# Kernel tuning notes

Measured on AMD Instinct MI355X. Metric: run time of the kernel, lower is better.

Reference implementation:

```python
import jax, jax.numpy as jnp
import numpy as np

INPUT_DIM = 768
HIDDEN_DIM = 256
ASPECT_NUM = 20
BATCH = 1024


def setup_inputs() -> dict:
    key = jax.random.key(0)
    k_x, k_w1, k_b1, k_w2, k_b2, k_id = jax.random.split(key, 6)
    X = jax.random.normal(k_x, (BATCH, INPUT_DIM), dtype=jnp.float32)
    aspect_ids = jax.random.randint(k_id, (BATCH,), 0, ASPECT_NUM, dtype=jnp.int64)
    # embedding tables (learned params), init like nn.Embedding (N(0,1))
    W1_embs = jax.random.normal(k_w1, (ASPECT_NUM, INPUT_DIM * HIDDEN_DIM), dtype=jnp.float32)
    b1_embs = jax.random.normal(k_b1, (ASPECT_NUM, HIDDEN_DIM), dtype=jnp.float32)
    W2_embs = jax.random.normal(k_w2, (ASPECT_NUM, HIDDEN_DIM * 2), dtype=jnp.float32)
    b2_embs = jax.random.normal(k_b2, (ASPECT_NUM, 2), dtype=jnp.float32)
    return {"X": X, "aspect_ids": aspect_ids, "W1_embs": W1_embs,
            "b1_embs": b1_embs, "W2_embs": W2_embs, "b2_embs": b2_embs}


def reference(X, aspect_ids, W1_embs, b1_embs, W2_embs, b2_embs):
    B = X.shape[0]
    # per-sample parameter gather (embedding lookup)
    W1 = W1_embs[aspect_ids].reshape(B, INPUT_DIM, HIDDEN_DIM)  # (B, D, H)
    b1 = b1_embs[aspect_ids]                                     # (B, H)
    W2 = W2_embs[aspect_ids].reshape(B, HIDDEN_DIM, 2)           # (B, H, 2)
    b2 = b2_embs[aspect_ids]                                     # (B, 2)
    # batched tiny 2-layer MLP
    out1 = jax.nn.relu(jnp.einsum('bd,bdh->bh', X, W1) + b1)     # (B, H)
    logits = jnp.einsum('bh,bht->bt', out1, W2) + b2             # (B, 2)
    return logits
```

## Files before the change

kernel.cpp:

```cpp
#include <hip/hip_runtime.h>


constexpr int D  = 768;
constexpr int H  = 256;
constexpr int NA = 20;
constexpr int NB = 1024;
constexpr int S  = 64;
constexpr int DKN = 8;
constexpr int KS  = D / DKN;
constexpr int HSN = 4;
constexpr int RW  = KS + 8;

constexpr size_t WS_NEEDED = (size_t)NB * DKN * H * 2;

typedef __attribute__((ext_vector_type(8))) short short8v;
typedef __attribute__((ext_vector_type(4))) float f32x4;

__device__ __forceinline__ unsigned f2bf(float x) {
    const unsigned u = __float_as_uint(x);
    return (u + 0x7FFFu + ((u >> 16) & 1u)) >> 16;
}
__device__ __forceinline__ float bflo(unsigned u) { return __uint_as_float(u << 16); }
__device__ __forceinline__ float bfhi(unsigned u) { return __uint_as_float(u & 0xFFFF0000u); }

__global__ __launch_bounds__(256, 4) void gemm1_kernel(
    const float* __restrict__ X,
    const int*   __restrict__ aids,
    const float* __restrict__ W1,
    const float* __restrict__ b1,
    unsigned short* __restrict__ part)
{
    __shared__ __align__(16) short w1t[64 * RW];
    __shared__ __align__(16) short xl[S * RW];
    __shared__ int sidx[NB + S];
    __shared__ int n_sh;

    const int t = threadIdx.x;
    const int w = t >> 6, l = t & 63;
    const int bid = blockIdx.x;
    const int hs  = bid / 160;
    const int p   = bid - hs * 160;
    const int aid = p % NA;
    const int dk  = p / NA;

    if (w == 0) {
        int run = 0;
        #pragma unroll
        for (int base = 0; base < NB; base += 256) {
            const int4 v = *reinterpret_cast<const int4*>(&aids[base + l * 4]);
            #pragma unroll
            for (int j = 0; j < 4; ++j) {
                const int id = (j == 0) ? v.x : (j == 1) ? v.y : (j == 2) ? v.z : v.w;
                const unsigned long long m = __ballot(id == aid);
                const int pre = run + __popcll(m & ((1ull << l) - 1));
                if (id == aid) sidx[pre] = base + l * 4 + j;
                run += __popcll(m);
            }
        }
        if (run > 0) {
            const int last = sidx[run - 1];
            const int npad = ((run + S - 1) / S) * S;
            if (run + l < npad) sidx[run + l] = last;
        }
        if (l == 0) n_sh = run;
    } else {
        const float* W1s = W1 + (size_t)aid * D * H + (size_t)dk * KS * H + hs * 64;
        unsigned* w1u = reinterpret_cast<unsigned*>(w1t);
        for (int i = t - 64; i < (KS / 2) * 16; i += 192) {
            const int kq = i >> 4, cq = i & 15;
            const int k0 = kq * 2;
            const float4 a = *reinterpret_cast<const float4*>(&W1s[(size_t)k0 * H + cq * 4]);
            const float4 b = *reinterpret_cast<const float4*>(&W1s[(size_t)(k0 + 1) * H + cq * 4]);
            w1u[(cq * 4 + 0) * (RW / 2) + kq] = f2bf(a.x) | (f2bf(b.x) << 16);
            w1u[(cq * 4 + 1) * (RW / 2) + kq] = f2bf(a.y) | (f2bf(b.y) << 16);
            w1u[(cq * 4 + 2) * (RW / 2) + kq] = f2bf(a.z) | (f2bf(b.z) << 16);
            w1u[(cq * 4 + 3) * (RW / 2) + kq] = f2bf(a.w) | (f2bf(b.w) << 16);
        }
    }
    __syncthreads();
    const int n = n_sh;
    if (n == 0) return;

    const int cg = l & 15, gq = l >> 4;
    const short* wa = &w1t[(w * 16 + cg) * RW + 8 * gq];
    const int gcol = hs * 64 + w * 16 + cg;
    const float b1v = (dk == 0) ? b1[(size_t)aid * H + gcol] : 0.f;

    for (int ch = 0; ch * S < n; ++ch) {
        for (int i = t; i < S * (KS / 4); i += 256) {
            const int r = i / (KS / 4), q = i - r * (KS / 4);
            const float4 v = *reinterpret_cast<const float4*>(
                &X[(size_t)sidx[ch * S + r] * D + dk * KS + q * 4]);
            uint2 o;
            o.x = f2bf(v.x) | (f2bf(v.y) << 16);
            o.y = f2bf(v.z) | (f2bf(v.w) << 16);
            *reinterpret_cast<uint2*>(&xl[r * RW + q * 4]) = o;
        }
        __syncthreads();

        f32x4 acc0 = {0,0,0,0}, acc1 = {0,0,0,0}, acc2 = {0,0,0,0}, acc3 = {0,0,0,0};
        #pragma unroll
        for (int ks = 0; ks < 3; ++ks) {
            const short8v bv = *reinterpret_cast<const short8v*>(wa + ks * 32);
            const int kof = ks * 32 + 8 * gq;
            acc0 = __builtin_amdgcn_mfma_f32_16x16x32_bf16(
                *reinterpret_cast<const short8v*>(&xl[(cg)      * RW + kof]), bv, acc0, 0, 0, 0);
            acc1 = __builtin_amdgcn_mfma_f32_16x16x32_bf16(
                *reinterpret_cast<const short8v*>(&xl[(16 + cg) * RW + kof]), bv, acc1, 0, 0, 0);
            acc2 = __builtin_amdgcn_mfma_f32_16x16x32_bf16(
                *reinterpret_cast<const short8v*>(&xl[(32 + cg) * RW + kof]), bv, acc2, 0, 0, 0);
            acc3 = __builtin_amdgcn_mfma_f32_16x16x32_bf16(
                *reinterpret_cast<const short8v*>(&xl[(48 + cg) * RW + kof]), bv, acc3, 0, 0, 0);
        }

        const int cv = min(S, n - ch * S);
        #pragma unroll
        for (int r = 0; r < 4; ++r) {
            const int s0 = gq * 4 + r;
            if (s0 < cv)
                part[((size_t)sidx[ch * S + s0] * DKN + dk) * H + gcol] =
                    (unsigned short)f2bf(acc0[r] + b1v);
            const int s1 = 16 + gq * 4 + r;
            if (s1 < cv)
                part[((size_t)sidx[ch * S + s1] * DKN + dk) * H + gcol] =
                    (unsigned short)f2bf(acc1[r] + b1v);
            const int s2 = 32 + gq * 4 + r;
            if (s2 < cv)
                part[((size_t)sidx[ch * S + s2] * DKN + dk) * H + gcol] =
                    (unsigned short)f2bf(acc2[r] + b1v);
            const int s3 = 48 + gq * 4 + r;
            if (s3 < cv)
                part[((size_t)sidx[ch * S + s3] * DKN + dk) * H + gcol] =
                    (unsigned short)f2bf(acc3[r] + b1v);
        }
        if ((ch + 1) * S < n) __syncthreads();
    }
}

__global__ __launch_bounds__(256) void finish_kernel(
    const int*            __restrict__ aids,
    const unsigned short* __restrict__ part,
    const float*          __restrict__ W2,
    const float*          __restrict__ b2,
    float*                __restrict__ out)
{
    const int w = threadIdx.x >> 6, l = threadIdx.x & 63;
    const int half = l >> 5;
    const int m = l & 31;
    const int s = blockIdx.x * 8 + w * 2 + half;
    const int aid = aids[s];

    const unsigned short* ps = part + (size_t)s * DKN * H + m * 8;
    float v[8] = {0, 0, 0, 0, 0, 0, 0, 0};
    #pragma unroll
    for (int dk = 0; dk < DKN; ++dk) {
        const uint4 r = *reinterpret_cast<const uint4*>(ps + dk * H);
        v[0] += bflo(r.x); v[1] += bfhi(r.x);
        v[2] += bflo(r.y); v[3] += bfhi(r.y);
        v[4] += bflo(r.z); v[5] += bfhi(r.z);
        v[6] += bflo(r.w); v[7] += bfhi(r.w);
    }

    const float4* W2v = reinterpret_cast<const float4*>(&W2[((size_t)aid * H + m * 8) * 2]);
    float p0 = 0.f, p1 = 0.f;
    #pragma unroll
    for (int c4 = 0; c4 < 4; ++c4) {
        const float4 wv = W2v[c4];
        const float o0 = fmaxf(v[c4 * 2 + 0], 0.f);
        const float o1 = fmaxf(v[c4 * 2 + 1], 0.f);
        p0 += o0 * wv.x + o1 * wv.z;
        p1 += o0 * wv.y + o1 * wv.w;
    }

    #pragma unroll
    for (int msk = 1; msk < 32; msk <<= 1) {
        p0 += __shfl_xor(p0, msk, 64);
        p1 += __shfl_xor(p1, msk, 64);
    }
    if (m == 0) {
        const float2 b2v = reinterpret_cast<const float2*>(b2)[aid];
        reinterpret_cast<float2*>(out)[s] = make_float2(p0 + b2v.x, p1 + b2v.y);
    }
}

__global__ __launch_bounds__(256, 4) void aspect_mlp_fallback(
    const float* __restrict__ X, const int* __restrict__ aspect_ids,
    const float* __restrict__ W1_embs, const float* __restrict__ b1_embs,
    const float* __restrict__ W2_embs, const float* __restrict__ b2_embs,
    float* __restrict__ out)
{
    __shared__ float xs[D];
    __shared__ float pl[4][H];
    __shared__ float red[4][2];
    const int b = blockIdx.x, t = threadIdx.x, w = t >> 6, l = t & 63;
    const int aid = aspect_ids[b];
    const float4* Xr = reinterpret_cast<const float4*>(X + (size_t)b * D);
    if (t < D / 4) reinterpret_cast<float4*>(xs)[t] = Xr[t];
    __syncthreads();
    const float4* W1v = reinterpret_cast<const float4*>(W1_embs + (size_t)aid * (D * H));
    float4 acc = make_float4(0.f, 0.f, 0.f, 0.f);
    const int d0 = w * (D / 4);
    for (int d = d0; d < d0 + D / 4; ++d) {
        const float xv = xs[d];
        const float4 wv = W1v[d * (H / 4) + l];
        acc.x = fmaf(xv, wv.x, acc.x); acc.y = fmaf(xv, wv.y, acc.y);
        acc.z = fmaf(xv, wv.z, acc.z); acc.w = fmaf(xv, wv.w, acc.w);
    }
    reinterpret_cast<float4*>(pl[w])[l] = acc;
    __syncthreads();
    const float o = fmaxf(pl[0][t] + pl[1][t] + pl[2][t] + pl[3][t] + b1_embs[aid * H + t], 0.f);
    const float2 w2 = reinterpret_cast<const float2*>(W2_embs)[aid * H + t];
    float p0 = o * w2.x, p1 = o * w2.y;
    for (int s = 32; s; s >>= 1) { p0 += __shfl_xor(p0, s, 64); p1 += __shfl_xor(p1, s, 64); }
    if (l == 0) { red[w][0] = p0; red[w][1] = p1; }
    __syncthreads();
    if (t == 0) {
        const float2 bias2 = reinterpret_cast<const float2*>(b2_embs)[aid];
        out[b * 2 + 0] = red[0][0] + red[1][0] + red[2][0] + red[3][0] + bias2.x;
        out[b * 2 + 1] = red[0][1] + red[1][1] + red[2][1] + red[3][1] + bias2.y;
    }
}

extern "C" void kernel_launch(void* const* d_in, const int* in_sizes, int n_in,
                              void* d_out, int out_size, void* d_ws, size_t ws_size,
                              hipStream_t stream) {
    const float* X          = (const float*)d_in[0];
    const int*   aspect_ids = (const int*)d_in[1];
    const float* W1_embs    = (const float*)d_in[2];
    const float* b1_embs    = (const float*)d_in[3];
    const float* W2_embs    = (const float*)d_in[4];
    const float* b2_embs    = (const float*)d_in[5];
    float*       out        = (float*)d_out;

    const int Brt = in_sizes[0] / D;
    const int na  = in_sizes[2] / (D * H);

    if (Brt != NB || na != NA || ws_size < WS_NEEDED) {
        aspect_mlp_fallback<<<Brt, 256, 0, stream>>>(
            X, aspect_ids, W1_embs, b1_embs, W2_embs, b2_embs, out);
        return;
    }

    unsigned short* part = (unsigned short*)d_ws;

    gemm1_kernel<<<NA * HSN * DKN, 256, 0, stream>>>(
        X, aspect_ids, W1_embs, b1_embs, part);
    finish_kernel<<<NB / 8, 256, 0, stream>>>(
        aspect_ids, part, W2_embs, b2_embs, out);
}
```

Measured before the change: 15.19 us.

## Retile gemm1 to fewer K splits and narrower 32-column H slices

Halves the number of K splits (8 to 4) and doubles the H slices (4 to 8), so each block covers 192 K values and 32 output columns. The four waves now split as 2 column tiles by 2 sample halves, replacing one column tile by four sample tiles. This halves the partial-sum workspace that finish_kernel must read and reduce, but the X tile in LDS is twice as large per block, so occupancy drops (launch bounds 4 to 3) and X is gathered once per H slice, eight times in total.

Measured after the change: 14.56 us. 1.04x faster.

```diff
diff --git a/kernel.cpp b/kernel.cpp
--- a/kernel.cpp
+++ b/kernel.cpp
@@ -6,9 +6,9 @@
 constexpr int NA = 20;
 constexpr int NB = 1024;
 constexpr int S  = 64;
-constexpr int DKN = 8;
+constexpr int DKN = 4;
 constexpr int KS  = D / DKN;
-constexpr int HSN = 4;
+constexpr int HSN = 8;
 constexpr int RW  = KS + 8;
 
 constexpr size_t WS_NEEDED = (size_t)NB * DKN * H * 2;
@@ -23,14 +23,14 @@
 __device__ __forceinline__ float bflo(unsigned u) { return __uint_as_float(u << 16); }
 __device__ __forceinline__ float bfhi(unsigned u) { return __uint_as_float(u & 0xFFFF0000u); }
 
-__global__ __launch_bounds__(256, 4) void gemm1_kernel(
+__global__ __launch_bounds__(256, 3) void gemm1_kernel(
     const float* __restrict__ X,
     const int*   __restrict__ aids,
     const float* __restrict__ W1,
     const float* __restrict__ b1,
     unsigned short* __restrict__ part)
 {
-    __shared__ __align__(16) short w1t[64 * RW];
+    __shared__ __align__(16) short w1t[32 * RW];
     __shared__ __align__(16) short xl[S * RW];
     __shared__ int sidx[NB + S];
     __shared__ int n_sh;
@@ -38,8 +38,8 @@
     const int t = threadIdx.x;
     const int w = t >> 6, l = t & 63;
     const int bid = blockIdx.x;
-    const int hs  = bid / 160;
-    const int p   = bid - hs * 160;
+    const int hs  = bid / 80;
+    const int p   = bid - hs * 80;
     const int aid = p % NA;
     const int dk  = p / NA;
 
@@ -64,10 +64,10 @@
         }
         if (l == 0) n_sh = run;
     } else {
-        const float* W1s = W1 + (size_t)aid * D * H + (size_t)dk * KS * H + hs * 64;
+        const float* W1s = W1 + (size_t)aid * D * H + (size_t)dk * KS * H + hs * 32;
         unsigned* w1u = reinterpret_cast<unsigned*>(w1t);
-        for (int i = t - 64; i < (KS / 2) * 16; i += 192) {
-            const int kq = i >> 4, cq = i & 15;
+        for (int i = t - 64; i < (KS / 2) * 8; i += 192) {
+            const int kq = i >> 3, cq = i & 7;
             const int k0 = kq * 2;
             const float4 a = *reinterpret_cast<const float4*>(&W1s[(size_t)k0 * H + cq * 4]);
             const float4 b = *reinterpret_cast<const float4*>(&W1s[(size_t)(k0 + 1) * H + cq * 4]);
@@ -82,8 +82,10 @@
     if (n == 0) return;
 
     const int cg = l & 15, gq = l >> 4;
-    const short* wa = &w1t[(w * 16 + cg) * RW + 8 * gq];
-    const int gcol = hs * 64 + w * 16 + cg;
+    const int ct = w & 1;
+    const int sh = w >> 1;
+    const short* wa = &w1t[(ct * 16 + cg) * RW + 8 * gq];
+    const int gcol = hs * 32 + ct * 16 + cg;
     const float b1v = (dk == 0) ? b1[(size_t)aid * H + gcol] : 0.f;
 
     for (int ch = 0; ch * S < n; ++ch) {
@@ -98,40 +100,28 @@
         }
         __syncthreads();
 
-        f32x4 acc0 = {0,0,0,0}, acc1 = {0,0,0,0}, acc2 = {0,0,0,0}, acc3 = {0,0,0,0};
+        f32x4 acc0 = {0,0,0,0}, acc1 = {0,0,0,0};
         #pragma unroll
-        for (int ks = 0; ks < 3; ++ks) {
+        for (int ks = 0; ks < KS / 32; ++ks) {
             const short8v bv = *reinterpret_cast<const short8v*>(wa + ks * 32);
             const int kof = ks * 32 + 8 * gq;
             acc0 = __builtin_amdgcn_mfma_f32_16x16x32_bf16(
-                *reinterpret_cast<const short8v*>(&xl[(cg)      * RW + kof]), bv, acc0, 0, 0, 0);
+                *reinterpret_cast<const short8v*>(&xl[(sh * 32 + cg)      * RW + kof]), bv, acc0, 0, 0, 0);
             acc1 = __builtin_amdgcn_mfma_f32_16x16x32_bf16(
-                *reinterpret_cast<const short8v*>(&xl[(16 + cg) * RW + kof]), bv, acc1, 0, 0, 0);
-            acc2 = __builtin_amdgcn_mfma_f32_16x16x32_bf16(
-                *reinterpret_cast<const short8v*>(&xl[(32 + cg) * RW + kof]), bv, acc2, 0, 0, 0);
-            acc3 = __builtin_amdgcn_mfma_f32_16x16x32_bf16(
-                *reinterpret_cast<const short8v*>(&xl[(48 + cg) * RW + kof]), bv, acc3, 0, 0, 0);
+                *reinterpret_cast<const short8v*>(&xl[(sh * 32 + 16 + cg) * RW + kof]), bv, acc1, 0, 0, 0);
         }
 
         const int cv = min(S, n - ch * S);
         #pragma unroll
         for (int r = 0; r < 4; ++r) {
-            const int s0 = gq * 4 + r;
+            const int s0 = sh * 32 + gq * 4 + r;
             if (s0 < cv)
                 part[((size_t)sidx[ch * S + s0] * DKN + dk) * H + gcol] =
                     (unsigned short)f2bf(acc0[r] + b1v);
-            const int s1 = 16 + gq * 4 + r;
+            const int s1 = sh * 32 + 16 + gq * 4 + r;
             if (s1 < cv)
                 part[((size_t)sidx[ch * S + s1] * DKN + dk) * H + gcol] =
                     (unsigned short)f2bf(acc1[r] + b1v);
-            const int s2 = 32 + gq * 4 + r;
-            if (s2 < cv)
-                part[((size_t)sidx[ch * S + s2] * DKN + dk) * H + gcol] =
-                    (unsigned short)f2bf(acc2[r] + b1v);
-            const int s3 = 48 + gq * 4 + r;
-            if (s3 < cv)
-                part[((size_t)sidx[ch * S + s3] * DKN + dk) * H + gcol] =
-                    (unsigned short)f2bf(acc3[r] + b1v);
         }
         if ((ch + 1) * S < n) __syncthreads();
     }
```
